# Kernel optimization log

Measured on AMD Instinct MI355X. Metric: run time of the kernel, lower is better.

Reference implementation:

```python
import jax, jax.numpy as jnp
import numpy as np

B, I, H = 4096, 1024, 1024


def setup_inputs() -> dict:
    key = jax.random.key(0)
    ks = jax.random.split(key, 22)
    def n(k, shape, scale=1.0):
        return jax.random.normal(k, shape, dtype=jnp.float32) * scale
    s = 0.02  # small init for weights to keep gates in sensitive range
    return {
        "x": n(ks[0], (B, I)),
        "h": n(ks[1], (B, H)),
        "c": n(ks[2], (B, H)),
        "W_ii_w": n(ks[3], (H, I), s), "W_ii_b": n(ks[4], (H,), s),
        "W_hi_w": n(ks[5], (H, H), s), "W_hi_b": n(ks[6], (H,), s),
        "W_ci":   n(ks[7], (H,), s),
        "W_if_w": n(ks[8], (H, I), s), "W_if_b": n(ks[9], (H,), s),
        "W_hf_w": n(ks[10], (H, H), s), "W_hf_b": n(ks[11], (H,), s),
        "W_cf":   n(ks[12], (H,), s),
        "W_ig_w": n(ks[13], (H, I), s), "W_ig_b": n(ks[14], (H,), s),
        "W_hg_w": n(ks[15], (H, H), s), "W_hg_b": n(ks[16], (H,), s),
        "W_io_w": n(ks[17], (H, I), s), "W_io_b": n(ks[18], (H,), s),
        "W_ho_w": n(ks[19], (H, H), s), "W_ho_b": n(ks[20], (H,), s),
        "W_co":   n(ks[21], (H,), s),
    }


def reference(x, h, c,
              W_ii_w, W_ii_b, W_hi_w, W_hi_b, W_ci,
              W_if_w, W_if_b, W_hf_w, W_hf_b, W_cf,
              W_ig_w, W_ig_b, W_hg_w, W_hg_b,
              W_io_w, W_io_b, W_ho_w, W_ho_b, W_co):
    # Fuse the 4 input projections and 4 hidden projections into single GEMMs.
    # Weight layout matches torch nn.Linear: y = x @ W.T + b
    Wx = jnp.concatenate([W_ii_w, W_if_w, W_ig_w, W_io_w], axis=0)  # [4H, I]
    Wh = jnp.concatenate([W_hi_w, W_hf_w, W_hg_w, W_ho_w], axis=0)  # [4H, H]
    bx = jnp.concatenate([W_ii_b, W_if_b, W_ig_b, W_io_b])          # [4H]
    bh = jnp.concatenate([W_hi_b, W_hf_b, W_hg_b, W_ho_b])          # [4H]
    z = x @ Wx.T + h @ Wh.T + (bx + bh)  # [B, 4H]
    zi, zf, zg, zo = jnp.split(z, 4, axis=-1)
    i = jax.nn.sigmoid(zi + W_ci * c)
    f = jax.nn.sigmoid(zf + W_cf * c)
    g = jnp.tanh(zg)
    c_next = f * c + i * g
    o = jax.nn.sigmoid(zo + W_co * c_next)
    h_next = o * jnp.tanh(c_next)
    return (h_next, c_next)
```

## Files before the change

kernel.cpp:

```cpp
#include <hip/hip_runtime.h>
#include <hip/hip_bf16.h>

#define BD 4096
#define ID 1024
#define HD 1024
#define KD 2048
#define ND 4096

typedef __attribute__((ext_vector_type(8))) __bf16 bf16x8;
typedef __attribute__((ext_vector_type(4))) float f32x4;

static __device__ __forceinline__ unsigned short f2bf(float f) {
  union { float f; unsigned u; } v; v.f = f;
  unsigned u = v.u;
  unsigned r = u + 0x7fffu + ((u >> 16) & 1u);
  return (unsigned short)(r >> 16);
}
static __device__ __forceinline__ float bf2f(unsigned short s) {
  union { unsigned u; float f; } v; v.u = ((unsigned)s) << 16;
  return v.f;
}

static __device__ __forceinline__ void gload_lds16(const void* g, void* l) {
  __builtin_amdgcn_global_load_lds(
      (const __attribute__((address_space(1))) void*)g,
      (__attribute__((address_space(3))) void*)l, 16, 0, 0);
}

static __device__ __forceinline__ float fast_sigmoid(float x) {
  return 1.0f / (1.0f + __expf(-x));
}
static __device__ __forceinline__ float fast_tanh(float x) {
  float t = __expf(-2.0f * fabsf(x));
  float r = (1.0f - t) / (1.0f + t);
  return copysignf(r, x);
}

__global__ void pack_A(const float* __restrict__ x, const float* __restrict__ h,
                       unsigned short* __restrict__ A) {
  int idx = blockIdx.x * blockDim.x + threadIdx.x;
  int e = idx << 2;
  int b = e >> 11;
  int k = e & 2047;
  const float* src = (k < ID) ? (x + (size_t)b * ID + k)
                              : (h + (size_t)b * HD + (k - ID));
  float4 v = *reinterpret_cast<const float4*>(src);
  ushort4 o;
  o.x = f2bf(v.x); o.y = f2bf(v.y); o.z = f2bf(v.z); o.w = f2bf(v.w);
  *reinterpret_cast<ushort4*>(A + e) = o;
}

__global__ void pack_B(const float* __restrict__ wxi, const float* __restrict__ wxf,
                       const float* __restrict__ wxg, const float* __restrict__ wxo,
                       const float* __restrict__ whi, const float* __restrict__ whf,
                       const float* __restrict__ whg, const float* __restrict__ who,
                       unsigned short* __restrict__ Bm) {
  int idx = blockIdx.x * blockDim.x + threadIdx.x;
  int e = idx << 2;
  int n = e >> 11;
  int k = e & 2047;
  int g = n >> 10, r = n & 1023;
  const float* src;
  if (k < ID) {
    src = (g == 0) ? wxi : (g == 1) ? wxf : (g == 2) ? wxg : wxo;
    src += (size_t)r * ID + k;
  } else {
    src = (g == 0) ? whi : (g == 1) ? whf : (g == 2) ? whg : who;
    src += (size_t)r * HD + (k - ID);
  }
  float4 v = *reinterpret_cast<const float4*>(src);
  ushort4 o;
  o.x = f2bf(v.x); o.y = f2bf(v.y); o.z = f2bf(v.z); o.w = f2bf(v.w);
  *reinterpret_cast<ushort4*>(Bm + e) = o;
}

__global__ __launch_bounds__(256, 2) void gemm_bf16(
    const unsigned short* __restrict__ A,
    const unsigned short* __restrict__ Bm,
    unsigned short* __restrict__ Z) {
  __shared__ __attribute__((aligned(16))) unsigned short As[128 * 32];
  __shared__ __attribute__((aligned(16))) unsigned short Bs[128 * 32];

  const int tid  = threadIdx.x;
  const int lane = tid & 63;
  const int w    = tid >> 6;
  const int wr   = w >> 1;
  const int wc   = w & 1;
  const int m0   = blockIdx.y * 128;
  const int n0   = blockIdx.x * 128;

  f32x4 acc[4][4];
#pragma unroll
  for (int i = 0; i < 4; ++i)
#pragma unroll
    for (int j = 0; j < 4; ++j)
      acc[i][j] = (f32x4){0.f, 0.f, 0.f, 0.f};

  const int chunk0 = w * 2;
  const int srow   = lane >> 2;
  const int skq    = (lane & 3) * 8;

  const unsigned short* gA0 = A  + (size_t)(m0 + chunk0 * 16 + srow) * KD + skq;
  const unsigned short* gA1 = A  + (size_t)(m0 + chunk0 * 16 + 16 + srow) * KD + skq;
  const unsigned short* gB0 = Bm + (size_t)(n0 + chunk0 * 16 + srow) * KD + skq;
  const unsigned short* gB1 = Bm + (size_t)(n0 + chunk0 * 16 + 16 + srow) * KD + skq;
  unsigned short* lA0 = &As[(chunk0 * 16) * 32];
  unsigned short* lA1 = &As[(chunk0 * 16 + 16) * 32];
  unsigned short* lB0 = &Bs[(chunk0 * 16) * 32];
  unsigned short* lB1 = &Bs[(chunk0 * 16 + 16) * 32];

  const int kq = (lane >> 4) * 8;
  const int rA = wr * 64 + (lane & 15);
  const int rB = wc * 64 + (lane & 15);

  for (int kt = 0; kt < KD; kt += 32) {
    gload_lds16(gA0 + kt, lA0);
    gload_lds16(gA1 + kt, lA1);
    gload_lds16(gB0 + kt, lB0);
    gload_lds16(gB1 + kt, lB1);
    __syncthreads();

    bf16x8 af[4], bfr[4];
#pragma unroll
    for (int mi = 0; mi < 4; ++mi)
      af[mi] = *(const bf16x8*)&As[(rA + mi * 16) * 32 + kq];
#pragma unroll
    for (int ni = 0; ni < 4; ++ni)
      bfr[ni] = *(const bf16x8*)&Bs[(rB + ni * 16) * 32 + kq];
#pragma unroll
    for (int mi = 0; mi < 4; ++mi)
#pragma unroll
      for (int ni = 0; ni < 4; ++ni)
        acc[mi][ni] = __builtin_amdgcn_mfma_f32_16x16x32_bf16(
            af[mi], bfr[ni], acc[mi][ni], 0, 0, 0);
    __syncthreads();
  }

  const int col0 = n0 + wc * 64 + (lane & 15);
  const int row0 = m0 + wr * 64 + (lane >> 4) * 4;
#pragma unroll
  for (int mi = 0; mi < 4; ++mi)
#pragma unroll
    for (int ni = 0; ni < 4; ++ni)
#pragma unroll
      for (int q = 0; q < 4; ++q) {
        int row = row0 + mi * 16 + q;
        int col = col0 + ni * 16;
        Z[(size_t)row * ND + col] = f2bf(acc[mi][ni][q]);
      }
}

__global__ void lstm_cell(const unsigned short* __restrict__ Z,
                          const float* __restrict__ c,
                          const float* __restrict__ bxi, const float* __restrict__ bhi,
                          const float* __restrict__ bxf, const float* __restrict__ bhf,
                          const float* __restrict__ bxg, const float* __restrict__ bhg,
                          const float* __restrict__ bxo, const float* __restrict__ bho,
                          const float* __restrict__ pci, const float* __restrict__ pcf,
                          const float* __restrict__ pco,
                          float* __restrict__ out) {
  int idx = blockIdx.x * blockDim.x + threadIdx.x;
  int e = idx << 2;
  int b = e >> 10;
  int r = e & 1023;
  const size_t zrow = (size_t)b * ND;

  ushort4 zi4 = *(const ushort4*)&Z[zrow + r];
  ushort4 zf4 = *(const ushort4*)&Z[zrow + 1024 + r];
  ushort4 zg4 = *(const ushort4*)&Z[zrow + 2048 + r];
  ushort4 zo4 = *(const ushort4*)&Z[zrow + 3072 + r];
  float4 c4   = *(const float4*)&c[e];
  float4 vbxi = *(const float4*)&bxi[r];
  float4 vbhi = *(const float4*)&bhi[r];
  float4 vbxf = *(const float4*)&bxf[r];
  float4 vbhf = *(const float4*)&bhf[r];
  float4 vbxg = *(const float4*)&bxg[r];
  float4 vbhg = *(const float4*)&bhg[r];
  float4 vbxo = *(const float4*)&bxo[r];
  float4 vbho = *(const float4*)&bho[r];
  float4 vpci = *(const float4*)&pci[r];
  float4 vpcf = *(const float4*)&pcf[r];
  float4 vpco = *(const float4*)&pco[r];

  unsigned short ziu[4] = {zi4.x, zi4.y, zi4.z, zi4.w};
  unsigned short zfu[4] = {zf4.x, zf4.y, zf4.z, zf4.w};
  unsigned short zgu[4] = {zg4.x, zg4.y, zg4.z, zg4.w};
  unsigned short zou[4] = {zo4.x, zo4.y, zo4.z, zo4.w};
  float cc[4]  = {c4.x, c4.y, c4.z, c4.w};
  float bi_[4] = {vbxi.x + vbhi.x, vbxi.y + vbhi.y, vbxi.z + vbhi.z, vbxi.w + vbhi.w};
  float bf_[4] = {vbxf.x + vbhf.x, vbxf.y + vbhf.y, vbxf.z + vbhf.z, vbxf.w + vbhf.w};
  float bg_[4] = {vbxg.x + vbhg.x, vbxg.y + vbhg.y, vbxg.z + vbhg.z, vbxg.w + vbhg.w};
  float bo_[4] = {vbxo.x + vbho.x, vbxo.y + vbho.y, vbxo.z + vbho.z, vbxo.w + vbho.w};
  float pi_[4] = {vpci.x, vpci.y, vpci.z, vpci.w};
  float pf_[4] = {vpcf.x, vpcf.y, vpcf.z, vpcf.w};
  float po_[4] = {vpco.x, vpco.y, vpco.z, vpco.w};

  float hn[4], cn[4];
#pragma unroll
  for (int j = 0; j < 4; ++j) {
    float vi = bf2f(ziu[j]) + bi_[j] + pi_[j] * cc[j];
    float vf = bf2f(zfu[j]) + bf_[j] + pf_[j] * cc[j];
    float vg = bf2f(zgu[j]) + bg_[j];
    float vo = bf2f(zou[j]) + bo_[j];
    float ig = fast_sigmoid(vi);
    float fg = fast_sigmoid(vf);
    float gg = fast_tanh(vg);
    float cnext = fg * cc[j] + ig * gg;
    float og = fast_sigmoid(vo + po_[j] * cnext);
    cn[j] = cnext;
    hn[j] = og * fast_tanh(cnext);
  }
  float4 ho = {hn[0], hn[1], hn[2], hn[3]};
  float4 co = {cn[0], cn[1], cn[2], cn[3]};
  *(float4*)&out[e] = ho;
  *(float4*)&out[(size_t)BD * HD + e] = co;
}

extern "C" void kernel_launch(void* const* d_in, const int* in_sizes, int n_in,
                              void* d_out, int out_size, void* d_ws, size_t ws_size,
                              hipStream_t stream) {
  const float* x      = (const float*)d_in[0];
  const float* h      = (const float*)d_in[1];
  const float* c      = (const float*)d_in[2];
  const float* W_ii_w = (const float*)d_in[3];
  const float* W_ii_b = (const float*)d_in[4];
  const float* W_hi_w = (const float*)d_in[5];
  const float* W_hi_b = (const float*)d_in[6];
  const float* W_ci   = (const float*)d_in[7];
  const float* W_if_w = (const float*)d_in[8];
  const float* W_if_b = (const float*)d_in[9];
  const float* W_hf_w = (const float*)d_in[10];
  const float* W_hf_b = (const float*)d_in[11];
  const float* W_cf   = (const float*)d_in[12];
  const float* W_ig_w = (const float*)d_in[13];
  const float* W_ig_b = (const float*)d_in[14];
  const float* W_hg_w = (const float*)d_in[15];
  const float* W_hg_b = (const float*)d_in[16];
  const float* W_io_w = (const float*)d_in[17];
  const float* W_io_b = (const float*)d_in[18];
  const float* W_ho_w = (const float*)d_in[19];
  const float* W_ho_b = (const float*)d_in[20];
  const float* W_co   = (const float*)d_in[21];

  unsigned short* Apack = (unsigned short*)d_ws;
  unsigned short* Bpack = Apack + (size_t)BD * KD;
  unsigned short* Zbuf  = Bpack + (size_t)ND * KD;
  float* out = (float*)d_out;

  dim3 blk(256);
  pack_A<<<dim3(8192), blk, 0, stream>>>(x, h, Apack);
  pack_B<<<dim3(8192), blk, 0, stream>>>(W_ii_w, W_if_w, W_ig_w, W_io_w,
                                         W_hi_w, W_hf_w, W_hg_w, W_ho_w, Bpack);
  gemm_bf16<<<dim3(32, 32), blk, 0, stream>>>(Apack, Bpack, Zbuf);
  lstm_cell<<<dim3(4096), blk, 0, stream>>>(Zbuf, c,
      W_ii_b, W_hi_b, W_if_b, W_hf_b, W_ig_b, W_hg_b, W_io_b, W_ho_b,
      W_ci, W_cf, W_co, out);
}
```

Baseline: 251.1 us.

## Retile GEMM to 256x256 double-buffered swizzled LDS and merge pack kernels

Replaces the 128x128, single-buffered GEMM with 256x256 tiles, 512 threads, a K-step of 64 and double-buffered LDS. Global-to-LDS loads use an XOR swizzle to avoid bank conflicts. The next tile's load overlaps the MFMAs, and the grid order is swizzled for L2 locality. The two pack kernels are merged into one launch. This cuts global traffic per flop and launch overhead, at the cost of 128KB of LDS per block, a large register footprint and only 256 blocks.

```diff
diff --git a/kernel.cpp b/kernel.cpp
--- a/kernel.cpp
+++ b/kernel.cpp
@@ -36,118 +36,145 @@
   return copysignf(r, x);
 }
 
-__global__ void pack_A(const float* __restrict__ x, const float* __restrict__ h,
-                       unsigned short* __restrict__ A) {
-  int idx = blockIdx.x * blockDim.x + threadIdx.x;
-  int e = idx << 2;
-  int b = e >> 11;
-  int k = e & 2047;
-  const float* src = (k < ID) ? (x + (size_t)b * ID + k)
-                              : (h + (size_t)b * HD + (k - ID));
-  float4 v = *reinterpret_cast<const float4*>(src);
-  ushort4 o;
-  o.x = f2bf(v.x); o.y = f2bf(v.y); o.z = f2bf(v.z); o.w = f2bf(v.w);
-  *reinterpret_cast<ushort4*>(A + e) = o;
-}
-
-__global__ void pack_B(const float* __restrict__ wxi, const float* __restrict__ wxf,
-                       const float* __restrict__ wxg, const float* __restrict__ wxo,
-                       const float* __restrict__ whi, const float* __restrict__ whf,
-                       const float* __restrict__ whg, const float* __restrict__ who,
-                       unsigned short* __restrict__ Bm) {
-  int idx = blockIdx.x * blockDim.x + threadIdx.x;
-  int e = idx << 2;
-  int n = e >> 11;
-  int k = e & 2047;
-  int g = n >> 10, r = n & 1023;
-  const float* src;
-  if (k < ID) {
-    src = (g == 0) ? wxi : (g == 1) ? wxf : (g == 2) ? wxg : wxo;
-    src += (size_t)r * ID + k;
+__global__ void pack_AB(const float* __restrict__ x, const float* __restrict__ h,
+                        const float* __restrict__ wxi, const float* __restrict__ wxf,
+                        const float* __restrict__ wxg, const float* __restrict__ wxo,
+                        const float* __restrict__ whi, const float* __restrict__ whf,
+                        const float* __restrict__ whg, const float* __restrict__ who,
+                        unsigned short* __restrict__ A, unsigned short* __restrict__ Bm) {
+  if (blockIdx.x < 8192) {
+    int idx = blockIdx.x * blockDim.x + threadIdx.x;
+    int e = idx << 2;
+    int b = e >> 11;
+    int k = e & 2047;
+    const float* src = (k < ID) ? (x + (size_t)b * ID + k)
+                                : (h + (size_t)b * HD + (k - ID));
+    float4 v = *reinterpret_cast<const float4*>(src);
+    ushort4 o;
+    o.x = f2bf(v.x); o.y = f2bf(v.y); o.z = f2bf(v.z); o.w = f2bf(v.w);
+    *reinterpret_cast<ushort4*>(A + e) = o;
   } else {
-    src = (g == 0) ? whi : (g == 1) ? whf : (g == 2) ? whg : who;
-    src += (size_t)r * HD + (k - ID);
+    int idx = (blockIdx.x - 8192) * blockDim.x + threadIdx.x;
+    int e = idx << 2;
+    int n = e >> 11;
+    int k = e & 2047;
+    int g = n >> 10, r = n & 1023;
+    const float* src;
+    if (k < ID) {
+      src = (g == 0) ? wxi : (g == 1) ? wxf : (g == 2) ? wxg : wxo;
+      src += (size_t)r * ID + k;
+    } else {
+      src = (g == 0) ? whi : (g == 1) ? whf : (g == 2) ? whg : who;
+      src += (size_t)r * HD + (k - ID);
+    }
+    float4 v = *reinterpret_cast<const float4*>(src);
+    ushort4 o;
+    o.x = f2bf(v.x); o.y = f2bf(v.y); o.z = f2bf(v.z); o.w = f2bf(v.w);
+    *reinterpret_cast<ushort4*>(Bm + e) = o;
   }
-  float4 v = *reinterpret_cast<const float4*>(src);
-  ushort4 o;
-  o.x = f2bf(v.x); o.y = f2bf(v.y); o.z = f2bf(v.z); o.w = f2bf(v.w);
-  *reinterpret_cast<ushort4*>(Bm + e) = o;
-}
-
-__global__ __launch_bounds__(256, 2) void gemm_bf16(
+}
+
+__global__ __launch_bounds__(512, 2) void gemm_bf16(
     const unsigned short* __restrict__ A,
     const unsigned short* __restrict__ Bm,
     unsigned short* __restrict__ Z) {
-  __shared__ __attribute__((aligned(16))) unsigned short As[128 * 32];
-  __shared__ __attribute__((aligned(16))) unsigned short Bs[128 * 32];
+  __shared__ __attribute__((aligned(16))) unsigned short lds[65536];
 
   const int tid  = threadIdx.x;
   const int lane = tid & 63;
   const int w    = tid >> 6;
-  const int wr   = w >> 1;
-  const int wc   = w & 1;
-  const int m0   = blockIdx.y * 128;
-  const int n0   = blockIdx.x * 128;
-
-  f32x4 acc[4][4];
-#pragma unroll
-  for (int i = 0; i < 4; ++i)
+  const int wr   = w >> 2;
+  const int wc   = w & 3;
+
+  const int bid = blockIdx.x;
+  const int swz = (bid & 7) * 32 + (bid >> 3);
+  const int m0  = (swz >> 4) * 256;
+  const int n0  = (swz & 15) * 256;
+
+  f32x4 acc[8][4];
+#pragma unroll
+  for (int i = 0; i < 8; ++i)
 #pragma unroll
     for (int j = 0; j < 4; ++j)
       acc[i][j] = (f32x4){0.f, 0.f, 0.f, 0.f};
 
-  const int chunk0 = w * 2;
-  const int srow   = lane >> 2;
-  const int skq    = (lane & 3) * 8;
-
-  const unsigned short* gA0 = A  + (size_t)(m0 + chunk0 * 16 + srow) * KD + skq;
-  const unsigned short* gA1 = A  + (size_t)(m0 + chunk0 * 16 + 16 + srow) * KD + skq;
-  const unsigned short* gB0 = Bm + (size_t)(n0 + chunk0 * 16 + srow) * KD + skq;
-  const unsigned short* gB1 = Bm + (size_t)(n0 + chunk0 * 16 + 16 + srow) * KD + skq;
-  unsigned short* lA0 = &As[(chunk0 * 16) * 32];
-  unsigned short* lA1 = &As[(chunk0 * 16 + 16) * 32];
-  unsigned short* lB0 = &Bs[(chunk0 * 16) * 32];
-  unsigned short* lB1 = &Bs[(chunk0 * 16 + 16) * 32];
-
-  const int kq = (lane >> 4) * 8;
-  const int rA = wr * 64 + (lane & 15);
-  const int rB = wc * 64 + (lane & 15);
-
-  for (int kt = 0; kt < KD; kt += 32) {
-    gload_lds16(gA0 + kt, lA0);
-    gload_lds16(gA1 + kt, lA1);
-    gload_lds16(gB0 + kt, lB0);
-    gload_lds16(gB1 + kt, lB1);
-    __syncthreads();
-
-    bf16x8 af[4], bfr[4];
-#pragma unroll
-    for (int mi = 0; mi < 4; ++mi)
-      af[mi] = *(const bf16x8*)&As[(rA + mi * 16) * 32 + kq];
+  const int sw  = lane & 7;
+  const int rA0 = (wr * 128 + (lane & 15)) * 64;
+  const int rB0 = (wc * 64  + (lane & 15)) * 64;
+  const int offk0 = (((lane >> 4)    ) ^ sw) * 8;
+  const int offk1 = (((lane >> 4) + 4) ^ sw) * 8;
+
+  unsigned short* ldsA = lds;
+  unsigned short* ldsB = lds + 32768;
+
+  auto stage = [&](int buf, int kt) {
+#pragma unroll
+    for (int j = 0; j < 4; ++j) {
+      int ci  = j * 512 + tid;
+      int row = ci >> 3;
+      int sc  = (ci & 7) ^ (row & 7);
+      const unsigned short* gA = A  + (size_t)(m0 + row) * KD + kt + sc * 8;
+      const unsigned short* gB = Bm + (size_t)(n0 + row) * KD + kt + sc * 8;
+      unsigned short* lA = ldsA + buf * 16384 + (j * 512 + (tid & ~63)) * 8;
+      unsigned short* lB = ldsB + buf * 16384 + (j * 512 + (tid & ~63)) * 8;
+      gload_lds16(gA, lA);
+      gload_lds16(gB, lB);
+    }
+  };
+
+  stage(0, 0);
+
+  for (int T = 0; T < 32; ++T) {
+    const int buf = T & 1;
+    const unsigned short* pA = ldsA + buf * 16384;
+    const unsigned short* pB = ldsB + buf * 16384;
+
+    asm volatile("s_waitcnt vmcnt(0)" ::: "memory");
+    __builtin_amdgcn_s_barrier();
+    __builtin_amdgcn_sched_barrier(0);
+
+    bf16x8 bfr[4][2];
+#pragma unroll
+    for (int ni = 0; ni < 4; ++ni) {
+      bfr[ni][0] = *(const bf16x8*)(pB + rB0 + ni * 1024 + offk0);
+      bfr[ni][1] = *(const bf16x8*)(pB + rB0 + ni * 1024 + offk1);
+    }
+
+    if (T < 31) stage(buf ^ 1, (T + 1) * 64);
+    __builtin_amdgcn_sched_barrier(0);
+
+#pragma unroll
+    for (int p = 0; p < 4; ++p) {
+      bf16x8 af[2][2];
+#pragma unroll
+      for (int i = 0; i < 2; ++i) {
+        af[i][0] = *(const bf16x8*)(pA + rA0 + (2 * p + i) * 1024 + offk0);
+        af[i][1] = *(const bf16x8*)(pA + rA0 + (2 * p + i) * 1024 + offk1);
+      }
+      __builtin_amdgcn_s_setprio(1);
+#pragma unroll
+      for (int i = 0; i < 2; ++i)
+#pragma unroll
+        for (int ni = 0; ni < 4; ++ni)
+#pragma unroll
+          for (int kk = 0; kk < 2; ++kk)
+            acc[2 * p + i][ni] = __builtin_amdgcn_mfma_f32_16x16x32_bf16(
+                af[i][kk], bfr[ni][kk], acc[2 * p + i][ni], 0, 0, 0);
+      __builtin_amdgcn_s_setprio(0);
+      __builtin_amdgcn_s_barrier();
+    }
+  }
+
+  const int col0 = n0 + wc * 64 + (lane & 15);
+  const int row0 = m0 + wr * 128 + (lane >> 4) * 4;
+#pragma unroll
+  for (int mi = 0; mi < 8; ++mi)
 #pragma unroll
     for (int ni = 0; ni < 4; ++ni)
-      bfr[ni] = *(const bf16x8*)&Bs[(rB + ni * 16) * 32 + kq];
-#pragma unroll
-    for (int mi = 0; mi < 4; ++mi)
-#pragma unroll
-      for (int ni = 0; ni < 4; ++ni)
-        acc[mi][ni] = __builtin_amdgcn_mfma_f32_16x16x32_bf16(
-            af[mi], bfr[ni], acc[mi][ni], 0, 0, 0);
-    __syncthreads();
-  }
-
-  const int col0 = n0 + wc * 64 + (lane & 15);
-  const int row0 = m0 + wr * 64 + (lane >> 4) * 4;
-#pragma unroll
-  for (int mi = 0; mi < 4; ++mi)
-#pragma unroll
-    for (int ni = 0; ni < 4; ++ni)
-#pragma unroll
-      for (int q = 0; q < 4; ++q) {
-        int row = row0 + mi * 16 + q;
-        int col = col0 + ni * 16;
-        Z[(size_t)row * ND + col] = f2bf(acc[mi][ni][q]);
-      }
+#pragma unroll
+      for (int q = 0; q < 4; ++q)
+        Z[(size_t)(row0 + mi * 16 + q) * ND + col0 + ni * 16] =
+            f2bf(acc[mi][ni][q]);
 }
 
 __global__ void lstm_cell(const unsigned short* __restrict__ Z,
@@ -247,12 +274,11 @@
   unsigned short* Zbuf  = Bpack + (size_t)ND * KD;
   float* out = (float*)d_out;
 
-  dim3 blk(256);
-  pack_A<<<dim3(8192), blk, 0, stream>>>(x, h, Apack);
-  pack_B<<<dim3(8192), blk, 0, stream>>>(W_ii_w, W_if_w, W_ig_w, W_io_w,
-                                         W_hi_w, W_hf_w, W_hg_w, W_ho_w, Bpack);
-  gemm_bf16<<<dim3(32, 32), blk, 0, stream>>>(Apack, Bpack, Zbuf);
-  lstm_cell<<<dim3(4096), blk, 0, stream>>>(Zbuf, c,
+  pack_AB<<<dim3(16384), dim3(256), 0, stream>>>(
+      x, h, W_ii_w, W_if_w, W_ig_w, W_io_w, W_hi_w, W_hf_w, W_hg_w, W_ho_w,
+      Apack, Bpack);
+  gemm_bf16<<<dim3(256), dim3(512), 0, stream>>>(Apack, Bpack, Zbuf);
+  lstm_cell<<<dim3(4096), dim3(256), 0, stream>>>(Zbuf, c,
       W_ii_b, W_hi_b, W_if_b, W_hf_b, W_ig_b, W_hg_b, W_io_b, W_ho_b,
       W_ci, W_cf, W_co, out);
 }
```

After: 234.9 us. -6.4%, faster.
